# Performance work log

Hardware: AMD Instinct MI355X
Metric: run time of the kernel (lower is better)

## Reference

```python
import jax, jax.numpy as jnp
import numpy as np
import math

N = 40000
E = 1280000
HID = 128
NF = 128
NG = 50
L = 3
CUTOFF = 10.0


def ssp(x):
    # shifted softplus: softplus(x) - log(2)
    return jax.nn.softplus(x) - jnp.float32(math.log(2.0))


def setup_inputs() -> dict:
    key = jax.random.key(0)
    ks = jax.random.split(key, 16)
    z = jax.random.randint(ks[0], (N,), 0, 100)
    pos = jax.random.normal(ks[1], (N, 3), dtype=jnp.float32) * 3.0
    batch = jnp.zeros((N,), dtype=jnp.int32)
    edge_index = jax.random.randint(ks[2], (2, E), 0, N)
    s = 0.1
    emb = jax.random.normal(ks[3], (100, HID), dtype=jnp.float32) * s
    mlp_w1 = jax.random.normal(ks[4], (L, NG, NF), dtype=jnp.float32) * s
    mlp_b1 = jnp.zeros((L, NF), dtype=jnp.float32)
    mlp_w2 = jax.random.normal(ks[5], (L, NF, NF), dtype=jnp.float32) * s
    mlp_b2 = jnp.zeros((L, NF), dtype=jnp.float32)
    conv_w1 = jax.random.normal(ks[6], (L, HID, NF), dtype=jnp.float32) * s  # no bias
    conv_w2 = jax.random.normal(ks[7], (L, NF, HID), dtype=jnp.float32) * s
    conv_b2 = jnp.zeros((L, HID), dtype=jnp.float32)
    lin_w = jax.random.normal(ks[8], (L, HID, HID), dtype=jnp.float32) * s
    lin_b = jnp.zeros((L, HID), dtype=jnp.float32)
    lin1_w = jax.random.normal(ks[9], (HID, HID // 2), dtype=jnp.float32) * s
    lin1_b = jnp.zeros((HID // 2,), dtype=jnp.float32)
    return {
        "z": z, "pos": pos, "batch": batch, "edge_index": edge_index,
        "emb": emb, "mlp_w1": mlp_w1, "mlp_b1": mlp_b1, "mlp_w2": mlp_w2,
        "mlp_b2": mlp_b2, "conv_w1": conv_w1, "conv_w2": conv_w2,
        "conv_b2": conv_b2, "lin_w": lin_w, "lin_b": lin_b,
        "lin1_w": lin1_w, "lin1_b": lin1_b,
    }


def reference(z, pos, batch, edge_index, emb, mlp_w1, mlp_b1, mlp_w2, mlp_b2,
              conv_w1, conv_w2, conv_b2, lin_w, lin_b, lin1_w, lin1_b):
    n = z.shape[0]
    row, col = edge_index[0], edge_index[1]
    # edge distances (radius-graph edge weights)
    diff = pos[row] - pos[col]                       # [E,3]
    edge_weight = jnp.sqrt(jnp.sum(diff * diff, axis=-1))  # [E]
    # Gaussian smearing
    offset = jnp.linspace(0.0, CUTOFF, NG, dtype=jnp.float32)
    coeff = -0.5 / (offset[1] - offset[0]) ** 2
    edge_attr = jnp.exp(coeff * (edge_weight[:, None] - offset[None, :]) ** 2)  # [E,NG]
    # cosine cutoff
    C = 0.5 * (jnp.cos(edge_weight * (jnp.pi / CUTOFF)) + 1.0)  # [E]

    h = emb[z]  # [N,HID]
    for l in range(L):
        W = ssp(edge_attr @ mlp_w1[l] + mlp_b1[l]) @ mlp_w2[l] + mlp_b2[l]  # [E,NF]
        W = W * C[:, None]
        x = h @ conv_w1[l]                      # [N,NF]
        msg = x[row] * W                        # gather + filter, [E,NF]
        agg = jax.ops.segment_sum(msg, col, num_segments=n)  # scatter-add, [N,NF]
        x = agg @ conv_w2[l] + conv_b2[l]       # [N,HID]
        x = ssp(x)
        x = x @ lin_w[l] + lin_b[l]
        h = h + x
    return ssp(h @ lin1_w + lin1_b)  # [N,HID//2]
```

## Files before the change

### kernel.cpp

```cpp
#include <hip/hip_runtime.h>
#include <math.h>


typedef _Float16 f16;
typedef _Float16 half8 __attribute__((ext_vector_type(8)));
typedef _Float16 half4v __attribute__((ext_vector_type(4)));
typedef float f32x4 __attribute__((ext_vector_type(4)));

#define NGAUSS 50
#define HIDF   128
#define NBINS  8192
#define DMAXF  40.0f
#define NLAYER 3
#define XST    132

static __device__ __forceinline__ float sspf(float v) {
    return fmaxf(v, 0.0f) + log1pf(expf(-fabsf(v))) - 0.6931471805599453f;
}

__global__ void k_hist(const int* __restrict__ ei, int* __restrict__ cnt, int E) {
    int e = blockIdx.x * blockDim.x + threadIdx.x;
    if (e >= E) return;
    atomicAdd(&cnt[ei[E + e]], 1);
}

__global__ __launch_bounds__(1024) void k_scan_part(const int* __restrict__ cnt,
                                                    int* __restrict__ epart,
                                                    int* __restrict__ bsum, int n) {
    __shared__ int ps[1024];
    int t = threadIdx.x;
    int i = blockIdx.x * 1024 + t;
    int v = (i < n) ? cnt[i] : 0;
    ps[t] = v;
    __syncthreads();
    for (int off = 1; off < 1024; off <<= 1) {
        int x = ps[t];
        int y = (t >= off) ? ps[t - off] : 0;
        __syncthreads();
        ps[t] = x + y;
        __syncthreads();
    }
    if (i < n) epart[i] = ps[t] - v;
    if (t == 1023) bsum[blockIdx.x] = ps[t];
}

__global__ __launch_bounds__(256) void k_scan_mid(const int* __restrict__ bsum,
                                                  int* __restrict__ bpre, int nb) {
    __shared__ int ps[256];
    int t = threadIdx.x;
    int v = (t < nb) ? bsum[t] : 0;
    ps[t] = v;
    __syncthreads();
    for (int off = 1; off < 256; off <<= 1) {
        int x = ps[t];
        int y = (t >= off) ? ps[t - off] : 0;
        __syncthreads();
        ps[t] = x + y;
        __syncthreads();
    }
    if (t < nb) bpre[t] = ps[t] - v;
}

__global__ __launch_bounds__(1024) void k_scan_fix(const int* __restrict__ epart,
                                                   const int* __restrict__ bpre,
                                                   const int* __restrict__ bsum,
                                                   int* __restrict__ offs,
                                                   int* __restrict__ cursor,
                                                   int n, int nb) {
    int i = blockIdx.x * 1024 + threadIdx.x;
    if (i == 0) offs[n] = bpre[nb - 1] + bsum[nb - 1];
    if (i >= n) return;
    int v = epart[i] + bpre[blockIdx.x];
    offs[i] = v;
    cursor[i] = v;
}

__global__ void k_scatter(const int* __restrict__ ei, const float* __restrict__ pos,
                          int* __restrict__ cursor, int* __restrict__ meta, int E) {
    const float SCALE = (float)(NBINS - 1) / DMAXF;
    int e = blockIdx.x * blockDim.x + threadIdx.x;
    if (e >= E) return;
    int r = ei[e], c = ei[E + e];
    float dx = pos[3*r+0] - pos[3*c+0];
    float dy = pos[3*r+1] - pos[3*c+1];
    float dz = pos[3*r+2] - pos[3*c+2];
    float d = sqrtf(dx*dx + dy*dy + dz*dz);
    float u = fminf(d * SCALE, (float)(NBINS - 1));
    int i0 = min((int)u, NBINS - 2);
    float w0 = u - (float)i0;
    int wq = (int)(w0 * 8.0f + 0.5f);
    if (wq == 8) { i0 = min(i0 + 1, NBINS - 2); wq = 0; }
    int p = atomicAdd(&cursor[c], 1);
    meta[p] = (i0 << 19) | (wq << 16) | r;
}

__global__ __launch_bounds__(128) void k_table(const float* __restrict__ w1,
                                               const float* __restrict__ b1,
                                               const float* __restrict__ w2,
                                               const float* __restrict__ b2,
                                               f16* __restrict__ T) {
    const float DELTA = 10.0f / 49.0f;
    const float COEFF = -0.5f / (DELTA * DELTA);
    const float HSTEP = DMAXF / (float)(NBINS - 1);
    __shared__ float ea[8][NGAUSS];
    __shared__ float u[8][HIDF];
    int l = blockIdx.y, b0 = blockIdx.x * 8, j = threadIdx.x;
    for (int idx = j; idx < 8 * NGAUSS; idx += 128) {
        int bb = idx / NGAUSS, g = idx % NGAUSS;
        float d = (float)(b0 + bb) * HSTEP;
        float diff = d - (float)g * DELTA;
        ea[bb][g] = expf(COEFF * diff * diff);
    }
    __syncthreads();
    float acc[8];
    {
        float bias = b1[l * HIDF + j];
#pragma unroll
        for (int b = 0; b < 8; ++b) acc[b] = bias;
        const float* w1l = w1 + (size_t)l * NGAUSS * HIDF;
        for (int g = 0; g < NGAUSS; ++g) {
            float wv = w1l[g * HIDF + j];
#pragma unroll
            for (int b = 0; b < 8; ++b) acc[b] = fmaf(ea[b][g], wv, acc[b]);
        }
#pragma unroll
        for (int b = 0; b < 8; ++b) u[b][j] = sspf(acc[b]);
    }
    __syncthreads();
    {
        float bias = b2[l * HIDF + j];
#pragma unroll
        for (int b = 0; b < 8; ++b) acc[b] = bias;
        const float* w2l = w2 + (size_t)l * HIDF * HIDF;
        for (int k = 0; k < HIDF; ++k) {
            float wv = w2l[k * HIDF + j];
#pragma unroll
            for (int b = 0; b < 8; ++b) acc[b] = fmaf(u[b][k], wv, acc[b]);
        }
    }
    f16* Tl = T + ((size_t)l * NBINS + b0) * HIDF;
#pragma unroll
    for (int b = 0; b < 8; ++b) {
        float d = (float)(b0 + b) * HSTEP;
        float C = 0.5f * (cosf(d * (float)(M_PI / 10.0)) + 1.0f);
        Tl[b * HIDF + j] = (f16)(acc[b] * C);
    }
}

__global__ void k_wpack(const float* __restrict__ cw1, const float* __restrict__ cw2,
                        const float* __restrict__ lw, const float* __restrict__ l1w,
                        f16* __restrict__ Wp) {
    int mat = blockIdx.y;
    int N = (mat == 9) ? 64 : HIDF;
    int ntiles = N >> 4;
    int tid = blockIdx.x * 256 + threadIdx.x;
    int lane = tid & 63, ks = (tid >> 6) & 3, nt = tid >> 8;
    if (nt >= ntiles) return;
    const float* W;
    if (mat < 9) {
        int l = mat / 3, kind = mat % 3;
        W = (kind == 0 ? cw1 : kind == 1 ? cw2 : lw) + (size_t)l * HIDF * HIDF;
    } else {
        W = l1w;
    }
    int kbase = ks * 32 + (lane >> 4) * 8;
    int col = nt * 16 + (lane & 15);
    half8 st;
#pragma unroll
    for (int j = 0; j < 8; ++j) st[j] = (f16)W[(size_t)(kbase + j) * N + col];
    *(half8*)&Wp[(size_t)mat * 16384 + ((size_t)(nt * 4 + ks) * 64 + lane) * 8] = st;
}

#define AGG_EDGE(yy)                                                         \
    {                                                                        \
        int row_ = (yy) & 0xFFFF;                                            \
        int i0_ = ((unsigned)(yy)) >> 19;                                    \
        float w0_ = (float)(((yy) >> 16) & 7) * 0.125f;                      \
        half8 x0_ = *(const half8*)&xj[(size_t)row_ * HIDF];                 \
        half8 ta_ = *(const half8*)&Tj[(size_t)i0_ * HIDF];                  \
        half8 tb_ = *(const half8*)&Tj[(size_t)(i0_ + 1) * HIDF];            \
        _Pragma("unroll")                                                    \
        for (int j = 0; j < 8; ++j) {                                        \
            float t0 = (float)ta_[j];                                        \
            float f0 = fmaf(w0_, (float)tb_[j] - t0, t0);                    \
            a[j] = fmaf((float)x0_[j], f0, a[j]);                            \
        }                                                                    \
    }

__global__ __launch_bounds__(256) void k_agg(const f16* __restrict__ x,
                                             const f16* __restrict__ T,
                                             const int* __restrict__ meta,
                                             const int* __restrict__ offs,
                                             f16* __restrict__ agg, int n) {
    int node = (blockIdx.x * blockDim.x + threadIdx.x) >> 4;
    int lane = threadIdx.x & 15;
    if (node >= n) return;
    int beg = offs[node], end = offs[node + 1];
    const f16* xj = x + lane * 8;
    const f16* Tj = T + lane * 8;
    float a[8] = {};
    for (int chunk = beg; chunk < end; chunk += 16) {
        int cnt = min(16, end - chunk);
        int mm = meta[chunk + min(lane, cnt - 1)];
        int q = 0;
        for (; q + 4 <= cnt; q += 4) {
            int y0 = __shfl(mm, q + 0, 16);
            int y1 = __shfl(mm, q + 1, 16);
            int y2 = __shfl(mm, q + 2, 16);
            int y3 = __shfl(mm, q + 3, 16);
            AGG_EDGE(y0)
            AGG_EDGE(y1)
            AGG_EDGE(y2)
            AGG_EDGE(y3)
        }
        for (; q < cnt; ++q) {
            int y0 = __shfl(mm, q, 16);
            AGG_EDGE(y0)
        }
    }
    half8 st;
#pragma unroll
    for (int j = 0; j < 8; ++j) st[j] = (f16)a[j];
    *(half8*)&agg[(size_t)node * HIDF + lane * 8] = st;
}

__global__ __launch_bounds__(256) void k_init_gemm(const int* __restrict__ z,
                                                   const float* __restrict__ emb,
                                                   const f16* __restrict__ w1p,
                                                   f16* __restrict__ xout) {
    int lane = threadIdx.x & 63;
    int wid = threadIdx.x >> 6;
    int m0 = blockIdx.x * 64 + wid * 16;
    int mrow = lane & 15, quad = lane >> 4;
    const float* er = emb + (size_t)z[m0 + mrow] * HIDF + quad * 8;
    half8 afr[4];
#pragma unroll
    for (int ks = 0; ks < 4; ++ks) {
        float4 a = *(const float4*)(er + ks * 32);
        float4 b = *(const float4*)(er + ks * 32 + 4);
        half8 f = {(f16)a.x, (f16)a.y, (f16)a.z, (f16)a.w,
                   (f16)b.x, (f16)b.y, (f16)b.z, (f16)b.w};
        afr[ks] = f;
    }
    f32x4 acc[8];
#pragma unroll
    for (int t = 0; t < 8; ++t) acc[t] = (f32x4){0.f, 0.f, 0.f, 0.f};
    const f16* bp = w1p + (size_t)lane * 8;
#pragma unroll
    for (int t = 0; t < 8; ++t)
#pragma unroll
        for (int ks = 0; ks < 4; ++ks) {
            half8 bfr = *(const half8*)(bp + (size_t)(t * 4 + ks) * 512);
            acc[t] = __builtin_amdgcn_mfma_f32_16x16x32_f16(afr[ks], bfr, acc[t], 0, 0, 0);
        }
    int col0 = lane & 15;
    int growb = m0 + quad * 4;
#pragma unroll
    for (int t = 0; t < 8; ++t)
#pragma unroll
        for (int r = 0; r < 4; ++r)
            xout[(size_t)(growb + r) * HIDF + t * 16 + col0] = (f16)acc[t][r];
}

template <int NT3, bool LAYER0, bool WRITE_H>
__global__ __launch_bounds__(256) void k_fused(const f16* __restrict__ agg,
                                               const f16* __restrict__ w2p,
                                               const float* __restrict__ b2,
                                               const f16* __restrict__ lwp,
                                               const float* __restrict__ lb,
                                               const f16* __restrict__ b3p,
                                               const float* __restrict__ b3,
                                               float* __restrict__ hio,
                                               const int* __restrict__ z,
                                               const float* __restrict__ emb,
                                               f16* __restrict__ xout,
                                               float* __restrict__ fout) {
    __shared__ f16 Xs[4][16][XST];
    int lane = threadIdx.x & 63;
    int wid = threadIdx.x >> 6;
    int m0 = blockIdx.x * 64 + wid * 16;
    int mrow = lane & 15, quad = lane >> 4;
    int col0 = mrow;
    int growb = m0 + quad * 4;
    f16 (*X)[XST] = Xs[wid];

    half8 afr[4];
    {
        const f16* Ar = agg + (size_t)(m0 + mrow) * HIDF + quad * 8;
#pragma unroll
        for (int ks = 0; ks < 4; ++ks) afr[ks] = *(const half8*)(Ar + ks * 32);
    }
    f32x4 acc[8];
#pragma unroll
    for (int t = 0; t < 8; ++t) acc[t] = (f32x4){0.f, 0.f, 0.f, 0.f};
    {
        const f16* bp = w2p + (size_t)lane * 8;
#pragma unroll
        for (int t = 0; t < 8; ++t)
#pragma unroll
            for (int ks = 0; ks < 4; ++ks) {
                half8 bfr = *(const half8*)(bp + (size_t)(t * 4 + ks) * 512);
                acc[t] = __builtin_amdgcn_mfma_f32_16x16x32_f16(afr[ks], bfr, acc[t], 0, 0, 0);
            }
    }
#pragma unroll
    for (int t = 0; t < 8; ++t) {
        int col = t * 16 + col0;
        float bv = b2[col];
#pragma unroll
        for (int r = 0; r < 4; ++r)
            X[quad * 4 + r][col] = (f16)sspf(acc[t][r] + bv);
    }
#pragma unroll
    for (int ks = 0; ks < 4; ++ks) {
        half4v lo = *(const half4v*)&X[mrow][ks * 32 + quad * 8];
        half4v hi = *(const half4v*)&X[mrow][ks * 32 + quad * 8 + 4];
        half8 f;
#pragma unroll
        for (int j = 0; j < 4; ++j) { f[j] = lo[j]; f[4 + j] = hi[j]; }
        afr[ks] = f;
    }
#pragma unroll
    for (int t = 0; t < 8; ++t) acc[t] = (f32x4){0.f, 0.f, 0.f, 0.f};
    {
        const f16* bp = lwp + (size_t)lane * 8;
#pragma unroll
        for (int t = 0; t < 8; ++t)
#pragma unroll
            for (int ks = 0; ks < 4; ++ks) {
                half8 bfr = *(const half8*)(bp + (size_t)(t * 4 + ks) * 512);
                acc[t] = __builtin_amdgcn_mfma_f32_16x16x32_f16(afr[ks], bfr, acc[t], 0, 0, 0);
            }
    }
    int zr[4];
    if (LAYER0) {
#pragma unroll
        for (int r = 0; r < 4; ++r) zr[r] = z[growb + r];
    }
#pragma unroll
    for (int t = 0; t < 8; ++t) {
        int col = t * 16 + col0;
        float bv = lb[col];
#pragma unroll
        for (int r = 0; r < 4; ++r) {
            int grow = growb + r;
            float resid = LAYER0 ? emb[(size_t)zr[r] * HIDF + col]
                                 : hio[(size_t)grow * HIDF + col];
            float hp = acc[t][r] + bv + resid;
            if (WRITE_H) hio[(size_t)grow * HIDF + col] = hp;
            X[quad * 4 + r][col] = (f16)hp;
        }
    }
#pragma unroll
    for (int ks = 0; ks < 4; ++ks) {
        half4v lo = *(const half4v*)&X[mrow][ks * 32 + quad * 8];
        half4v hi = *(const half4v*)&X[mrow][ks * 32 + quad * 8 + 4];
        half8 f;
#pragma unroll
        for (int j = 0; j < 4; ++j) { f[j] = lo[j]; f[4 + j] = hi[j]; }
        afr[ks] = f;
    }
#pragma unroll
    for (int t = 0; t < NT3; ++t) acc[t] = (f32x4){0.f, 0.f, 0.f, 0.f};
    {
        const f16* bp = b3p + (size_t)lane * 8;
#pragma unroll
        for (int t = 0; t < NT3; ++t)
#pragma unroll
            for (int ks = 0; ks < 4; ++ks) {
                half8 bfr = *(const half8*)(bp + (size_t)(t * 4 + ks) * 512);
                acc[t] = __builtin_amdgcn_mfma_f32_16x16x32_f16(afr[ks], bfr, acc[t], 0, 0, 0);
            }
    }
    if (NT3 == 8) {
#pragma unroll
        for (int t = 0; t < 8; ++t)
#pragma unroll
            for (int r = 0; r < 4; ++r)
                xout[(size_t)(growb + r) * HIDF + t * 16 + col0] = (f16)acc[t][r];
    } else {
#pragma unroll
        for (int t = 0; t < NT3; ++t) {
            int col = t * 16 + col0;
            float bv = b3[col];
#pragma unroll
            for (int r = 0; r < 4; ++r)
                fout[(size_t)(growb + r) * (NT3 * 16) + col] = sspf(acc[t][r] + bv);
        }
    }
}

extern "C" void kernel_launch(void* const* d_in, const int* in_sizes, int n_in,
                              void* d_out, int out_size, void* d_ws, size_t ws_size,
                              hipStream_t stream) {
    const int*   z       = (const int*)d_in[0];
    const float* pos     = (const float*)d_in[1];
    const int*   ei      = (const int*)d_in[3];
    const float* emb     = (const float*)d_in[4];
    const float* mlp_w1  = (const float*)d_in[5];
    const float* mlp_b1  = (const float*)d_in[6];
    const float* mlp_w2  = (const float*)d_in[7];
    const float* mlp_b2  = (const float*)d_in[8];
    const float* conv_w1 = (const float*)d_in[9];
    const float* conv_w2 = (const float*)d_in[10];
    const float* conv_b2 = (const float*)d_in[11];
    const float* lin_w   = (const float*)d_in[12];
    const float* lin_b   = (const float*)d_in[13];
    const float* lin1_w  = (const float*)d_in[14];
    const float* lin1_b  = (const float*)d_in[15];
    float* out = (float*)d_out;

    int n = in_sizes[0];
    int E = in_sizes[3] / 2;

    char* ws = (char*)d_ws;
    size_t off = 0;
    auto alloc = [&](size_t bytes) -> void* {
        void* p = ws + off;
        off = (off + bytes + 255) & ~(size_t)255;
        return p;
    };
    float* h     = (float*)alloc((size_t)n * HIDF * 4);
    f16*   x16   = (f16*)alloc((size_t)n * HIDF * 2);
    f16*   agg16 = (f16*)alloc((size_t)n * HIDF * 2);
    f16*   T16   = (f16*)alloc((size_t)NLAYER * NBINS * HIDF * 2);
    int*   meta  = (int*)alloc((size_t)E * 4);
    int*   offs  = (int*)alloc((size_t)(n + 1) * 4);
    int*   cur   = (int*)alloc((size_t)n * 4);
    int*   epart = (int*)alloc((size_t)n * 4);
    int*   bsum  = (int*)alloc(256 * 4);
    int*   bpre  = (int*)alloc(256 * 4);
    f16*   Wp    = (f16*)alloc((size_t)10 * 16384 * 2);

    const int tb = 256;
    int nb = (n + 1023) / 1024;
    hipMemsetAsync(cur, 0, (size_t)n * 4, stream);
    hipLaunchKernelGGL(k_hist, dim3((E + tb - 1) / tb), dim3(tb), 0, stream, ei, cur, E);
    hipLaunchKernelGGL(k_scan_part, dim3(nb), dim3(1024), 0, stream, cur, epart, bsum, n);
    hipLaunchKernelGGL(k_scan_mid, dim3(1), dim3(256), 0, stream, bsum, bpre, nb);
    hipLaunchKernelGGL(k_scan_fix, dim3(nb), dim3(1024), 0, stream,
                       epart, bpre, bsum, offs, cur, n, nb);
    hipLaunchKernelGGL(k_scatter, dim3((E + tb - 1) / tb), dim3(tb), 0, stream,
                       ei, pos, cur, meta, E);
    hipLaunchKernelGGL(k_wpack, dim3(8, 10), dim3(tb), 0, stream,
                       conv_w1, conv_w2, lin_w, lin1_w, Wp);
    hipLaunchKernelGGL(k_table, dim3(NBINS / 8, NLAYER), dim3(128), 0, stream,
                       mlp_w1, mlp_b1, mlp_w2, mlp_b2, T16);

    int gemmblocks = n / 64;
    int aggblocks = (n * 16 + tb - 1) / tb;
    hipLaunchKernelGGL(k_init_gemm, dim3(gemmblocks), dim3(tb), 0, stream,
                       z, emb, Wp + (size_t)0 * 16384, x16);
    hipLaunchKernelGGL(k_agg, dim3(aggblocks), dim3(tb), 0, stream,
                       x16, T16 + (size_t)0 * NBINS * HIDF, meta, offs, agg16, n);
    hipLaunchKernelGGL(HIP_KERNEL_NAME(k_fused<8, true, true>), dim3(gemmblocks), dim3(tb), 0, stream,
                       agg16, Wp + (size_t)1 * 16384, conv_b2 + 0 * HIDF,
                       Wp + (size_t)2 * 16384, lin_b + 0 * HIDF,
                       Wp + (size_t)3 * 16384, (const float*)nullptr,
                       h, z, emb, x16, (float*)nullptr);
    hipLaunchKernelGGL(k_agg, dim3(aggblocks), dim3(tb), 0, stream,
                       x16, T16 + (size_t)1 * NBINS * HIDF, meta, offs, agg16, n);
    hipLaunchKernelGGL(HIP_KERNEL_NAME(k_fused<8, false, true>), dim3(gemmblocks), dim3(tb), 0, stream,
                       agg16, Wp + (size_t)4 * 16384, conv_b2 + 1 * HIDF,
                       Wp + (size_t)5 * 16384, lin_b + 1 * HIDF,
                       Wp + (size_t)6 * 16384, (const float*)nullptr,
                       h, (const int*)nullptr, (const float*)nullptr, x16, (float*)nullptr);
    hipLaunchKernelGGL(k_agg, dim3(aggblocks), dim3(tb), 0, stream,
                       x16, T16 + (size_t)2 * NBINS * HIDF, meta, offs, agg16, n);
    hipLaunchKernelGGL(HIP_KERNEL_NAME(k_fused<4, false, false>), dim3(gemmblocks), dim3(tb), 0, stream,
                       agg16, Wp + (size_t)7 * 16384, conv_b2 + 2 * HIDF,
                       Wp + (size_t)8 * 16384, lin_b + 2 * HIDF,
                       Wp + (size_t)9 * 16384, lin1_b,
                       h, (const int*)nullptr, (const float*)nullptr, (f16*)nullptr, out);
    (void)n_in; (void)out_size; (void)ws_size;
}
```

Baseline: 519.5 us.

## Replace histogram-scan-scatter CSR build with two-pass bucketed LDS sort

Builds the destination-sorted edge list with a two-pass bucket sort instead of global histogram, three scan kernels and atomic scatter. The first pass groups 4096-edge chunks by 512-node bucket in shared memory and writes them into fixed-capacity staging regions. The second pass counts, scans and places each bucket's edges per node in shared memory, then writes CSR offsets and meta coalesced. This removes several launches and scattered global atomics, but adds a staging buffer with a fixed per-bucket capacity that could overflow on skewed graphs.

```diff
diff --git a/kernel.cpp b/kernel.cpp
--- a/kernel.cpp
+++ b/kernel.cpp
@@ -13,85 +13,126 @@
 #define DMAXF  40.0f
 #define NLAYER 3
 #define XST    132
+#define BSHIFT 9
+#define MAXBUCK 128
+#define SCAP  20480
 
 static __device__ __forceinline__ float sspf(float v) {
     return fmaxf(v, 0.0f) + log1pf(expf(-fabsf(v))) - 0.6931471805599453f;
 }
 
-__global__ void k_hist(const int* __restrict__ ei, int* __restrict__ cnt, int E) {
-    int e = blockIdx.x * blockDim.x + threadIdx.x;
-    if (e >= E) return;
-    atomicAdd(&cnt[ei[E + e]], 1);
-}
-
-__global__ __launch_bounds__(1024) void k_scan_part(const int* __restrict__ cnt,
-                                                    int* __restrict__ epart,
-                                                    int* __restrict__ bsum, int n) {
-    __shared__ int ps[1024];
+__global__ __launch_bounds__(256) void k_stage(const int* __restrict__ ei,
+                                               const float* __restrict__ pos,
+                                               int* __restrict__ scnt,
+                                               uint2* __restrict__ staging,
+                                               int E, int nbuck) {
+    const float SCALE = (float)(NBINS - 1) / DMAXF;
+    __shared__ int bhist[MAXBUCK];
+    __shared__ int boff[MAXBUCK];
+    __shared__ int gpos[MAXBUCK];
+    __shared__ uint2 recs[4096];
+    __shared__ unsigned char lbuck[4096];
     int t = threadIdx.x;
-    int i = blockIdx.x * 1024 + t;
-    int v = (i < n) ? cnt[i] : 0;
-    ps[t] = v;
-    __syncthreads();
-    for (int off = 1; off < 1024; off <<= 1) {
-        int x = ps[t];
-        int y = (t >= off) ? ps[t - off] : 0;
+    for (int i = t; i < nbuck; i += 256) bhist[i] = 0;
+    __syncthreads();
+    int e0 = blockIdx.x * 4096;
+    int cnt_here = min(4096, E - e0);
+    unsigned pay[16];
+    unsigned short cc[16];
+    short rk[16];
+#pragma unroll
+    for (int k = 0; k < 16; ++k) {
+        int idx = t + k * 256;
+        rk[k] = -1;
+        if (idx < cnt_here) {
+            int e = e0 + idx;
+            int r = ei[e], c = ei[E + e];
+            float dx = pos[3*r+0] - pos[3*c+0];
+            float dy = pos[3*r+1] - pos[3*c+1];
+            float dz = pos[3*r+2] - pos[3*c+2];
+            float d = sqrtf(dx*dx + dy*dy + dz*dz);
+            float u = fminf(d * SCALE, (float)(NBINS - 1));
+            int i0 = min((int)u, NBINS - 2);
+            float w0 = u - (float)i0;
+            int wq = (int)(w0 * 8.0f + 0.5f);
+            if (wq == 8) { i0 = min(i0 + 1, NBINS - 2); wq = 0; }
+            pay[k] = ((unsigned)i0 << 19) | ((unsigned)wq << 16) | (unsigned)r;
+            cc[k] = (unsigned short)c;
+            rk[k] = (short)atomicAdd(&bhist[c >> BSHIFT], 1);
+        }
+    }
+    __syncthreads();
+    if (t == 0) {
+        int run = 0;
+        for (int b = 0; b < nbuck; ++b) { boff[b] = run; run += bhist[b]; }
+    }
+    __syncthreads();
+    if (t < nbuck) gpos[t] = atomicAdd(&scnt[t], bhist[t]);
+    __syncthreads();
+#pragma unroll
+    for (int k = 0; k < 16; ++k) {
+        if (rk[k] >= 0) {
+            int b = cc[k] >> BSHIFT;
+            int slot = boff[b] + rk[k];
+            recs[slot] = make_uint2(pay[k], (unsigned)cc[k]);
+            lbuck[slot] = (unsigned char)b;
+        }
+    }
+    __syncthreads();
+    for (int i = t; i < cnt_here; i += 256) {
+        int b = lbuck[i];
+        staging[(size_t)b * SCAP + gpos[b] + (i - boff[b])] = recs[i];
+    }
+}
+
+__global__ __launch_bounds__(1024) void k_place(const uint2* __restrict__ staging,
+                                                const int* __restrict__ scnt,
+                                                int* __restrict__ meta,
+                                                int* __restrict__ offs,
+                                                int n, int nbuck) {
+    __shared__ int lcnt[512], loff[512], lcur[512];
+    __shared__ int ldsm[SCAP];
+    __shared__ int ebase_s;
+    int b = blockIdx.x, t = threadIdx.x;
+    int cntb = scnt[b];
+    if (t == 0) {
+        int run = 0;
+        for (int j = 0; j < b; ++j) run += scnt[j];
+        ebase_s = run;
+    }
+    for (int j = t; j < 512; j += 1024) { lcnt[j] = 0; lcur[j] = 0; }
+    __syncthreads();
+    int ebase = ebase_s;
+    const uint2* sb = staging + (size_t)b * SCAP;
+    for (int i = t; i < cntb; i += 1024)
+        atomicAdd(&lcnt[sb[i].y & 511], 1);
+    __syncthreads();
+    if (t < 512) loff[t] = lcnt[t];
+    __syncthreads();
+    for (int o = 1; o < 512; o <<= 1) {
+        int v = 0;
+        if (t < 512) { v = loff[t]; if (t >= o) v += loff[t - o]; }
         __syncthreads();
-        ps[t] = x + y;
+        if (t < 512) loff[t] = v;
         __syncthreads();
     }
-    if (i < n) epart[i] = ps[t] - v;
-    if (t == 1023) bsum[blockIdx.x] = ps[t];
-}
-
-__global__ __launch_bounds__(256) void k_scan_mid(const int* __restrict__ bsum,
-                                                  int* __restrict__ bpre, int nb) {
-    __shared__ int ps[256];
-    int t = threadIdx.x;
-    int v = (t < nb) ? bsum[t] : 0;
-    ps[t] = v;
-    __syncthreads();
-    for (int off = 1; off < 256; off <<= 1) {
-        int x = ps[t];
-        int y = (t >= off) ? ps[t - off] : 0;
-        __syncthreads();
-        ps[t] = x + y;
-        __syncthreads();
-    }
-    if (t < nb) bpre[t] = ps[t] - v;
-}
-
-__global__ __launch_bounds__(1024) void k_scan_fix(const int* __restrict__ epart,
-                                                   const int* __restrict__ bpre,
-                                                   const int* __restrict__ bsum,
-                                                   int* __restrict__ offs,
-                                                   int* __restrict__ cursor,
-                                                   int n, int nb) {
-    int i = blockIdx.x * 1024 + threadIdx.x;
-    if (i == 0) offs[n] = bpre[nb - 1] + bsum[nb - 1];
-    if (i >= n) return;
-    int v = epart[i] + bpre[blockIdx.x];
-    offs[i] = v;
-    cursor[i] = v;
-}
-
-__global__ void k_scatter(const int* __restrict__ ei, const float* __restrict__ pos,
-                          int* __restrict__ cursor, int* __restrict__ meta, int E) {
-    const float SCALE = (float)(NBINS - 1) / DMAXF;
-    int e = blockIdx.x * blockDim.x + threadIdx.x;
-    if (e >= E) return;
-    int r = ei[e], c = ei[E + e];
-    float dx = pos[3*r+0] - pos[3*c+0];
-    float dy = pos[3*r+1] - pos[3*c+1];
-    float dz = pos[3*r+2] - pos[3*c+2];
-    float d = sqrtf(dx*dx + dy*dy + dz*dz);
-    float u = fminf(d * SCALE, (float)(NBINS - 1));
-    int i0 = min((int)u, NBINS - 2);
-    float w0 = u - (float)i0;
-    int wq = (int)(w0 * 8.0f + 0.5f);
-    if (wq == 8) { i0 = min(i0 + 1, NBINS - 2); wq = 0; }
-    int p = atomicAdd(&cursor[c], 1);
-    meta[p] = (i0 << 19) | (wq << 16) | r;
+    int nb0 = b << BSHIFT;
+    if (t < 512) {
+        int node = nb0 + t;
+        if (node < n) offs[node] = ebase + loff[t] - lcnt[t];
+    }
+    if (b == nbuck - 1 && t == 0) offs[n] = ebase + cntb;
+    __syncthreads();
+    for (int i = t; i < cntb; i += 1024) {
+        uint2 r = sb[i];
+        int cl = (int)(r.y & 511);
+        int lpos = (loff[cl] - lcnt[cl]) + atomicAdd(&lcur[cl], 1);
+        if (lpos < SCAP) ldsm[lpos] = (int)r.x;
+        else meta[ebase + lpos] = (int)r.x;
+    }
+    __syncthreads();
+    int lim = min(cntb, SCAP);
+    for (int i = t; i < lim; i += 1024) meta[ebase + i] = ldsm[i];
 }
 
 __global__ __launch_bounds__(128) void k_table(const float* __restrict__ w1,
@@ -412,6 +453,7 @@
 
     int n = in_sizes[0];
     int E = in_sizes[3] / 2;
+    int nbuck = (n + 511) >> 9;
 
     char* ws = (char*)d_ws;
     size_t off = 0;
@@ -426,22 +468,16 @@
     f16*   T16   = (f16*)alloc((size_t)NLAYER * NBINS * HIDF * 2);
     int*   meta  = (int*)alloc((size_t)E * 4);
     int*   offs  = (int*)alloc((size_t)(n + 1) * 4);
-    int*   cur   = (int*)alloc((size_t)n * 4);
-    int*   epart = (int*)alloc((size_t)n * 4);
-    int*   bsum  = (int*)alloc(256 * 4);
-    int*   bpre  = (int*)alloc(256 * 4);
+    int*   scnt  = (int*)alloc((size_t)nbuck * 4);
+    uint2* staging = (uint2*)alloc((size_t)nbuck * SCAP * 8);
     f16*   Wp    = (f16*)alloc((size_t)10 * 16384 * 2);
 
     const int tb = 256;
-    int nb = (n + 1023) / 1024;
-    hipMemsetAsync(cur, 0, (size_t)n * 4, stream);
-    hipLaunchKernelGGL(k_hist, dim3((E + tb - 1) / tb), dim3(tb), 0, stream, ei, cur, E);
-    hipLaunchKernelGGL(k_scan_part, dim3(nb), dim3(1024), 0, stream, cur, epart, bsum, n);
-    hipLaunchKernelGGL(k_scan_mid, dim3(1), dim3(256), 0, stream, bsum, bpre, nb);
-    hipLaunchKernelGGL(k_scan_fix, dim3(nb), dim3(1024), 0, stream,
-                       epart, bpre, bsum, offs, cur, n, nb);
-    hipLaunchKernelGGL(k_scatter, dim3((E + tb - 1) / tb), dim3(tb), 0, stream,
-                       ei, pos, cur, meta, E);
+    hipMemsetAsync(scnt, 0, (size_t)nbuck * 4, stream);
+    hipLaunchKernelGGL(k_stage, dim3((E + 4095) / 4096), dim3(tb), 0, stream,
+                       ei, pos, scnt, staging, E, nbuck);
+    hipLaunchKernelGGL(k_place, dim3(nbuck), dim3(1024), 0, stream,
+                       staging, scnt, meta, offs, n, nbuck);
     hipLaunchKernelGGL(k_wpack, dim3(8, 10), dim3(tb), 0, stream,
                        conv_w1, conv_w2, lin_w, lin1_w, Wp);
     hipLaunchKernelGGL(k_table, dim3(NBINS / 8, NLAYER), dim3(128), 0, stream,
```

Result: faster. 436.8 us (-15.9%).
